# Optimization experiments

Measured on AMD Instinct MI355X. Metric: run time of the kernel, lower is better.

Reference implementation:

```python
import jax, jax.numpy as jnp
import numpy as np

B, S, D = 4, 4096, 1024
E, K, H = 8, 2, 2048


def setup_inputs() -> dict:
    key = jax.random.key(0)
    ks = jax.random.split(key, 6)
    scale_g = 1.0 / np.sqrt(D)
    scale_1 = 1.0 / np.sqrt(D)
    scale_2 = 1.0 / np.sqrt(H)
    return {
        "x": jax.random.normal(ks[0], (B, S, D), dtype=jnp.float32),
        "Wg": jax.random.uniform(ks[1], (D, E), jnp.float32, -scale_g, scale_g),
        "W1": jax.random.uniform(ks[2], (E, D, H), jnp.float32, -scale_1, scale_1),
        "b1": jax.random.uniform(ks[3], (E, H), jnp.float32, -scale_1, scale_1),
        "W2": jax.random.uniform(ks[4], (E, H, D), jnp.float32, -scale_2, scale_2),
        "b2": jax.random.uniform(ks[5], (E, D), jnp.float32, -scale_2, scale_2),
    }


def reference(x, Wg, W1, b1, W2, b2):
    # Router: softmax gate, top-k selection, renormalized combine weights
    logits = jnp.einsum("bsd,de->bse", x, Wg)          # [B,S,E]
    probs = jax.nn.softmax(logits, axis=-1)
    topv, topi = jax.lax.top_k(probs, K)                # [B,S,K]
    cw = topv / (jnp.sum(topv, axis=-1, keepdims=True) + 1e-9)
    # Per-token weight for each expert: sum over k of one_hot(idx_k)*cw_k -> [B,S,E]
    we = jnp.sum(jax.nn.one_hot(topi, E, dtype=x.dtype) * cw[..., None], axis=-2)
    # Weighted combine of per-expert FFN outputs (loop over small fixed E)
    y = jnp.zeros_like(x)
    for e in range(E):
        h = jax.nn.relu(jnp.einsum("bsd,dh->bsh", x, W1[e]) + b1[e])
        out_e = jnp.einsum("bsh,hd->bsd", h, W2[e]) + b2[e]
        y = y + we[..., e:e + 1] * out_e
    return y
```

## Files before the change

kernel.cpp:

```cpp
#include <hip/hip_runtime.h>
#include <hip/hip_bf16.h>

#define TOK 16384
#define DIM 1024
#define HID 2048
#define NEXP 8

typedef __attribute__((ext_vector_type(4))) float f32x4;
typedef __attribute__((ext_vector_type(8))) short s16x8;

__device__ __forceinline__ unsigned short f2bf(float f) {
  union { float f; unsigned u; } v; v.f = f;
  unsigned r = v.u + 0x7fffu + ((v.u >> 16) & 1u);
  return (unsigned short)(r >> 16);
}
__device__ __forceinline__ int tile_byte(int r, int kk2) {
  return (r * 128 + kk2) ^ ((r & 7) << 4);
}
__device__ __forceinline__ void gld_lds16(const void* g, void* l) {
  __builtin_amdgcn_global_load_lds(
      (const __attribute__((address_space(1))) unsigned int*)g,
      (__attribute__((address_space(3))) unsigned int*)l, 16, 0, 0);
}
__device__ __forceinline__ int xcd_swz(int p, int nwg) {
  int q = nwg >> 3, r = nwg & 7;
  int xcd = p & 7, idx = p >> 3;
  return (xcd < r ? xcd * (q + 1) : r * (q + 1) + (xcd - r) * q) + idx;
}

__global__ void wg_tr(const float* __restrict__ Wg, float* __restrict__ WgT) {
  int i = blockIdx.x * 256 + threadIdx.x;
  int e = i >> 10, dd = i & 1023;
  WgT[i] = Wg[dd * NEXP + e];
}

__global__ void prep_tiles(const float* __restrict__ src, unsigned short* __restrict__ dst,
                           int rows, int cols) {
  int ct = blockIdx.x, kb = blockIdx.y, e = blockIdx.z;
  int nct = gridDim.x, nkb = gridDim.y;
  __shared__ __align__(16) unsigned short tile[8192];
  const float* s = src + ((size_t)e * rows + kb * 64) * cols + ct * 128;
  int tid = threadIdx.x;
  #pragma unroll
  for (int it = 0; it < 8; it++) {
    int idx = it * 256 + tid;
    int kk = idx >> 5;
    int r4 = (idx & 31) * 4;
    float4 v = *(const float4*)(s + (size_t)kk * cols + r4);
    char* tb = (char*)tile;
    *(unsigned short*)(tb + tile_byte(r4 + 0, kk * 2)) = f2bf(v.x);
    *(unsigned short*)(tb + tile_byte(r4 + 1, kk * 2)) = f2bf(v.y);
    *(unsigned short*)(tb + tile_byte(r4 + 2, kk * 2)) = f2bf(v.z);
    *(unsigned short*)(tb + tile_byte(r4 + 3, kk * 2)) = f2bf(v.w);
  }
  __syncthreads();
  unsigned short* d = dst + (((size_t)e * nct + ct) * nkb + kb) * 8192;
  #pragma unroll
  for (int it = 0; it < 4; it++) {
    int o = it * 256 + tid;
    *(s16x8*)(d + o * 8) = *(const s16x8*)((const char*)tile + o * 16);
  }
}

__global__ __launch_bounds__(256)
void router_logits_cvt(const float* __restrict__ x, const float* __restrict__ WgT,
                       unsigned short* __restrict__ xbf,
                       int* __restrict__ sel, float2* __restrict__ wp) {
  int wave = threadIdx.x >> 6, lane = threadIdx.x & 63;
  int t = blockIdx.x * 4 + wave;
  const f32x4* xr = (const f32x4*)(x + (size_t)t * DIM);
  unsigned short* xb = xbf + (size_t)t * DIM;
  float acc[NEXP];
  #pragma unroll
  for (int e = 0; e < NEXP; e++) acc[e] = 0.f;
  #pragma unroll
  for (int q = 0; q < 4; q++) {
    f32x4 xv = xr[q * 64 + lane];
    ushort4 bv;
    bv.x = f2bf(xv[0]); bv.y = f2bf(xv[1]); bv.z = f2bf(xv[2]); bv.w = f2bf(xv[3]);
    *(ushort4*)(xb + (q * 64 + lane) * 4) = bv;
    #pragma unroll
    for (int e = 0; e < NEXP; e++) {
      f32x4 wv = *(const f32x4*)(WgT + (size_t)e * DIM + (q * 64 + lane) * 4);
      acc[e] = fmaf(xv[3], wv[3], fmaf(xv[2], wv[2], fmaf(xv[1], wv[1], fmaf(xv[0], wv[0], acc[e]))));
    }
  }
  #pragma unroll
  for (int e = 0; e < NEXP; e++) {
    float v = acc[e];
    #pragma unroll
    for (int off = 32; off >= 1; off >>= 1) v += __shfl_xor(v, off);
    acc[e] = v;
  }
  if (lane == 0) {
    float m = acc[0];
    #pragma unroll
    for (int e = 1; e < NEXP; e++) m = fmaxf(m, acc[e]);
    float p[NEXP], s = 0.f;
    #pragma unroll
    for (int e = 0; e < NEXP; e++) { p[e] = expf(acc[e] - m); s += p[e]; }
    float inv = 1.f / s;
    int i0 = 0; float v0 = p[0];
    #pragma unroll
    for (int e = 1; e < NEXP; e++) if (p[e] > v0) { v0 = p[e]; i0 = e; }
    int i1 = -1; float v1 = -1.f;
    #pragma unroll
    for (int e = 0; e < NEXP; e++) if (e != i0 && p[e] > v1) { v1 = p[e]; i1 = e; }
    v0 *= inv; v1 *= inv;
    float den = v0 + v1 + 1e-9f;
    sel[t] = i0 | (i1 << 4);
    wp[t] = make_float2(v0 / den, v1 / den);
  }
}

__global__ __launch_bounds__(256)
void router_scatter(const int* __restrict__ sel, const float2* __restrict__ wp,
                    int* __restrict__ counts, int* __restrict__ tok_list,
                    float* __restrict__ w_list) {
  __shared__ int lh0[4][16], lh1[4][16];
  __shared__ int bbase[16];
  int tid = threadIdx.x, wave = tid >> 6, lane = tid & 63;
  int t = blockIdx.x * 256 + tid;
  int s = sel[t];
  int b0 = s & 15;
  int b1 = 8 + ((s >> 4) & 15);
  float2 w = wp[t];
  unsigned long long lt = (lane == 63) ? ~0ull >> 1 : (((unsigned long long)1 << lane) - 1);
  int r0 = 0, r1 = 0;
  #pragma unroll
  for (int b = 0; b < 8; b++) {
    unsigned long long m0 = __ballot(b0 == b);
    if (b0 == b) r0 = __popcll(m0 & lt);
    if (lane == 0) { lh0[wave][b] = __popcll(m0); lh1[wave][b] = 0; }
  }
  #pragma unroll
  for (int b = 8; b < 16; b++) {
    unsigned long long m1 = __ballot(b1 == b);
    if (b1 == b) r1 = __popcll(m1 & lt);
    if (lane == 0) { lh1[wave][b] = __popcll(m1); lh0[wave][b] = 0; }
  }
  __syncthreads();
  if (tid < 16) {
    int h = 0;
    #pragma unroll
    for (int v = 0; v < 4; v++) h += lh0[v][tid] + lh1[v][tid];
    bbase[tid] = atomicAdd(&counts[tid], h);
  }
  __syncthreads();
  int p0 = bbase[b0] + r0;
  int p1 = bbase[b1] + r1;
  #pragma unroll
  for (int v = 0; v < 4; v++) {
    if (v < wave) { p0 += lh0[v][b0]; p1 += lh1[v][b1]; }
  }
  int e0 = b0, e1 = b1 - 8;
  tok_list[e0 * TOK + p0] = t;
  w_list[e0 * TOK + p0] = w.x;
  int q1 = TOK - 1 - p1;
  tok_list[e1 * TOK + q1] = t;
  w_list[e1 * TOK + q1] = w.y;
}

__global__ void calc_off(const int* __restrict__ counts, int* __restrict__ off) {
  if (threadIdx.x == 0 && blockIdx.x == 0) {
    int a = 0;
    for (int e = 0; e < NEXP; e++)
      for (int s = 0; s < 2; s++) {
        off[e * 2 + s] = a;
        a += (counts[s * 8 + e] + 127) & ~127;
      }
  }
}

__global__ __launch_bounds__(256, 4)
void moe_gemm1(const unsigned short* __restrict__ xbf, const unsigned short* __restrict__ w1s,
               const float* __restrict__ b1, const int* __restrict__ counts,
               const int* __restrict__ off, const int* __restrict__ tok_list,
               unsigned short* __restrict__ h_s, int ct_off, int nkbc, int nct) {
  int logical = xcd_swz(blockIdx.x, gridDim.x);
  int CG = (nct >= 8) ? 8 : nct;
  int e = -1, seg = 0, rt = 0, ct_l = 0, segcnt = 0, base = 0;
  #pragma unroll
  for (int zz = 0; zz < 16; zz++) {
    int ee = zz >> 1, ss = zz & 1;
    int c = counts[ss * 8 + ee];
    int nt = (c + 127) >> 7;
    int span = nt * nct;
    if (e < 0 && logical < base + span) {
      e = ee; seg = ss; segcnt = c;
      int local = logical - base;
      int grp = nt * CG;
      int h = local / grp, rem = local - h * grp;
      rt = rem / CG;
      ct_l = h * CG + (rem - rt * CG);
    }
    base += span;
  }
  if (e < 0) return;

  __shared__ __align__(16) unsigned short As[8192];
  __shared__ __align__(16) unsigned short Bs[8192];
  __shared__ int tokS[128];

  int tid = threadIdx.x, wave = tid >> 6, lane = tid & 63;
  int llo = lane & 15, lhi = lane >> 4;
  int wr = wave >> 1, wc = wave & 1;
  int ct_g = ct_off + ct_l;

  if (tid < 128) {
    int q = rt * 128 + tid;
    int qq = q < segcnt ? q : segcnt - 1;
    int slot = seg ? (TOK - 1 - qq) : qq;
    tokS[tid] = tok_list[e * TOK + slot];
  }
  __syncthreads();

  const char* srcA[4];
  #pragma unroll
  for (int i = 0; i < 4; i++) {
    int r = i * 32 + (tid >> 3);
    srcA[i] = (const char*)xbf + (size_t)tokS[r] * (DIM * 2) + (((tid & 7) ^ (r & 7)) * 16);
  }
  const char* gB = (const char*)(w1s + (((size_t)e * 16 + ct_g) * 16) * 8192);

  f32x4 acc[4][4];
  #pragma unroll
  for (int i = 0; i < 4; i++)
    #pragma unroll
    for (int j = 0; j < 4; j++) acc[i][j] = (f32x4){0.f, 0.f, 0.f, 0.f};

  for (int kb = 0; kb < 16; kb++) {
    #pragma unroll
    for (int i = 0; i < 4; i++)
      gld_lds16(srcA[i] + kb * 128, (char*)As + i * 4096 + wave * 1024);
    const char* gs = gB + (size_t)kb * 16384 + wave * 1024 + lane * 16;
    #pragma unroll
    for (int i = 0; i < 4; i++)
      gld_lds16(gs + i * 4096, (char*)Bs + i * 4096 + wave * 1024);
    __syncthreads();
    #pragma unroll
    for (int ks = 0; ks < 2; ks++) {
      s16x8 a[4], b[4];
      #pragma unroll
      for (int f = 0; f < 4; f++) {
        a[f] = *(const s16x8*)((const char*)As + tile_byte(wr * 64 + f * 16 + llo, ks * 64 + lhi * 16));
        b[f] = *(const s16x8*)((const char*)Bs + tile_byte(wc * 64 + f * 16 + llo, ks * 64 + lhi * 16));
      }
      #pragma unroll
      for (int fr = 0; fr < 4; fr++)
        #pragma unroll
        for (int fc = 0; fc < 4; fc++)
          acc[fr][fc] = __builtin_amdgcn_mfma_f32_16x16x32_bf16(a[fr], b[fc], acc[fr][fc], 0, 0, 0);
    }
    __syncthreads();
  }

  size_t grt = (size_t)(off[e * 2 + seg] >> 7) + rt;
  unsigned short* hb = h_s + grt * ((size_t)nkbc * 8192);
  const float* b1e = b1 + e * HID + ct_g * 128;
  #pragma unroll
  for (int fc = 0; fc < 4; fc++) {
    int col = wc * 64 + fc * 16 + llo;
    float bv = b1e[col];
    char* tb = (char*)(hb + ((size_t)(ct_l * 2 + (col >> 6))) * 8192);
    int kk2 = (col & 63) * 2;
    #pragma unroll
    for (int fr = 0; fr < 4; fr++) {
      int r0 = wr * 64 + fr * 16 + lhi * 4;
      #pragma unroll
      for (int j = 0; j < 4; j++) {
        float v = fmaxf(acc[fr][fc][j] + bv, 0.f);
        *(unsigned short*)(tb + tile_byte(r0 + j, kk2)) = f2bf(v);
      }
    }
  }
}

template<int NKBC>
__global__ __launch_bounds__(256, 4)
void moe_gemm2(const unsigned short* __restrict__ h_s, const unsigned short* __restrict__ w2s,
               const float* __restrict__ b2, const int* __restrict__ counts,
               const int* __restrict__ off, const int* __restrict__ tok_list,
               const float* __restrict__ w_list, float* __restrict__ y,
               int seg, int kb_off, int add_b2, int accum) {
  int logical = xcd_swz(blockIdx.x, gridDim.x);
  int e = -1, rt = 0, ct = 0, segcnt = 0, base = 0;
  #pragma unroll
  for (int ee = 0; ee < 8; ee++) {
    int c = counts[seg * 8 + ee];
    int nt = (c + 127) >> 7;
    int span = nt * 8;
    if (e < 0 && logical < base + span) {
      e = ee; segcnt = c;
      int local = logical - base;
      int grp = nt * 4;
      int h = local / grp, rem = local - h * grp;
      rt = rem >> 2;
      ct = h * 4 + (rem & 3);
    }
    base += span;
  }
  if (e < 0) return;

  __shared__ __align__(16) unsigned short As[8192];
  __shared__ __align__(16) unsigned short Bs[8192];

  int tid = threadIdx.x, wave = tid >> 6, lane = tid & 63;
  int llo = lane & 15, lhi = lane >> 4;
  int wr = wave >> 1, wc = wave & 1;

  size_t grt = (size_t)(off[e * 2 + seg] >> 7) + rt;
  const char* gA = (const char*)(h_s + grt * ((size_t)NKBC * 8192));
  const char* gB = (const char*)(w2s + (((size_t)e * 8 + ct) * 32 + kb_off) * 8192);

  f32x4 acc[4][4];
  #pragma unroll
  for (int i = 0; i < 4; i++)
    #pragma unroll
    for (int j = 0; j < 4; j++) acc[i][j] = (f32x4){0.f, 0.f, 0.f, 0.f};

  for (int kb = 0; kb < NKBC; kb++) {
    const char* ga = gA + (size_t)kb * 16384 + wave * 1024 + lane * 16;
    const char* gb = gB + (size_t)kb * 16384 + wave * 1024 + lane * 16;
    #pragma unroll
    for (int i = 0; i < 4; i++) {
      gld_lds16(ga + i * 4096, (char*)As + i * 4096 + wave * 1024);
      gld_lds16(gb + i * 4096, (char*)Bs + i * 4096 + wave * 1024);
    }
    __syncthreads();
    #pragma unroll
    for (int ks = 0; ks < 2; ks++) {
      s16x8 a[4], b[4];
      #pragma unroll
      for (int f = 0; f < 4; f++) {
        a[f] = *(const s16x8*)((const char*)As + tile_byte(wr * 64 + f * 16 + llo, ks * 64 + lhi * 16));
        b[f] = *(const s16x8*)((const char*)Bs + tile_byte(wc * 64 + f * 16 + llo, ks * 64 + lhi * 16));
      }
      #pragma unroll
      for (int fr = 0; fr < 4; fr++)
        #pragma unroll
        for (int fc = 0; fc < 4; fc++)
          acc[fr][fc] = __builtin_amdgcn_mfma_f32_16x16x32_bf16(a[fr], b[fc], acc[fr][fc], 0, 0, 0);
    }
    __syncthreads();
  }

  const float* b2e = b2 + e * DIM + ct * 128;
  #pragma unroll
  for (int fr = 0; fr < 4; fr++) {
    #pragma unroll
    for (int j = 0; j < 4; j++) {
      int q = rt * 128 + wr * 64 + fr * 16 + lhi * 4 + j;
      if (q < segcnt) {
        int slot = seg ? (TOK - 1 - q) : q;
        int t = tok_list[e * TOK + slot];
        float w = w_list[e * TOK + slot];
        float bs = add_b2 ? w : 0.f;
        #pragma unroll
        for (int fc = 0; fc < 4; fc++) {
          int col = wc * 64 + fc * 16 + llo;
          float val = w * acc[fr][fc][j] + bs * b2e[col];
          size_t idx = (size_t)t * DIM + ct * 128 + col;
          if (accum) y[idx] += val;
          else       y[idx] = val;
        }
      }
    }
  }
}

__global__ void transpose_cvt(const float* __restrict__ src, unsigned short* __restrict__ dst,
                              int R, int C) {
  __shared__ float tile[32][33];
  int e = blockIdx.z;
  const float* s = src + (size_t)e * R * C;
  unsigned short* d = dst + (size_t)e * R * C;
  int c0 = blockIdx.x * 32, r0 = blockIdx.y * 32;
  int tx = threadIdx.x, ty = threadIdx.y;
  #pragma unroll
  for (int i = 0; i < 32; i += 8)
    tile[ty + i][tx] = s[(size_t)(r0 + ty + i) * C + c0 + tx];
  __syncthreads();
  #pragma unroll
  for (int i = 0; i < 32; i += 8)
    d[(size_t)(c0 + ty + i) * R + r0 + tx] = f2bf(tile[tx][ty + i]);
}

__global__ void router_kernel(const float* __restrict__ x, const float* __restrict__ Wg,
                              int* __restrict__ counts, int* __restrict__ tok_list,
                              float* __restrict__ w_list) {
  int wave = threadIdx.x >> 6, lane = threadIdx.x & 63;
  int t = blockIdx.x * 4 + wave;
  const float* xr = x + (size_t)t * DIM;
  float acc[NEXP];
  #pragma unroll
  for (int e = 0; e < NEXP; e++) acc[e] = 0.f;
  for (int i = 0; i < DIM / 64; i++) {
    int dd = i * 64 + lane;
    float xv = xr[dd];
    const float* wr = Wg + (size_t)dd * NEXP;
    #pragma unroll
    for (int e = 0; e < NEXP; e++) acc[e] = fmaf(xv, wr[e], acc[e]);
  }
  #pragma unroll
  for (int e = 0; e < NEXP; e++) {
    float v = acc[e];
    #pragma unroll
    for (int off = 32; off >= 1; off >>= 1) v += __shfl_xor(v, off);
    acc[e] = v;
  }
  if (lane == 0) {
    float m = acc[0];
    #pragma unroll
    for (int e = 1; e < NEXP; e++) m = fmaxf(m, acc[e]);
    float p[NEXP], s = 0.f;
    #pragma unroll
    for (int e = 0; e < NEXP; e++) { p[e] = expf(acc[e] - m); s += p[e]; }
    float inv = 1.f / s;
    int i0 = 0; float v0 = p[0];
    #pragma unroll
    for (int e = 1; e < NEXP; e++) if (p[e] > v0) { v0 = p[e]; i0 = e; }
    int i1 = -1; float v1 = -1.f;
    #pragma unroll
    for (int e = 0; e < NEXP; e++) if (e != i0 && p[e] > v1) { v1 = p[e]; i1 = e; }
    v0 *= inv; v1 *= inv;
    float den = v0 + v1 + 1e-9f;
    float w0 = v0 / den, w1 = v1 / den;
    int q0 = atomicAdd(&counts[i0], 1);
    tok_list[i0 * TOK + q0] = t;           w_list[i0 * TOK + q0] = w0;
    int q1 = atomicAdd(&counts[8 + i1], 1);
    int p1 = TOK - 1 - q1;
    tok_list[i1 * TOK + p1] = t;           w_list[i1 * TOK + p1] = w1;
  }
}

__global__ __launch_bounds__(512, 4)
void moe_ffn_kernel(const float* __restrict__ x,
                    const unsigned short* __restrict__ w1t,
                    const unsigned short* __restrict__ w2t,
                    const float* __restrict__ b1, const float* __restrict__ b2,
                    const int* __restrict__ counts, const int* __restrict__ tok_list,
                    const float* __restrict__ w_list, float* __restrict__ y) {
  int zz = blockIdx.y, e = zz & 7, seg = zz >> 3;
  int segcnt = counts[seg * 8 + e];
  int row0 = blockIdx.x * 32;
  if (row0 >= segcnt) return;
  __shared__ unsigned short Xs[32 * DIM];
  __shared__ unsigned short hsl[32 * 64];
  __shared__ int tokS[32];
  __shared__ float wS[32];
  int tid = threadIdx.x, wave = tid >> 6, lane = tid & 63;
  if (tid < 32) {
    int q = row0 + tid;
    if (q < segcnt) {
      int slot = seg ? (TOK - 1 - q) : q;
      tokS[tid] = tok_list[e * TOK + slot]; wS[tid] = w_list[e * TOK + slot];
    } else { tokS[tid] = -1; wS[tid] = 0.f; }
  }
  __syncthreads();
  #pragma unroll
  for (int it = 0; it < 8; it++) {
    int chunk = it * 512 + tid;
    int r = chunk >> 7, c = (chunk & 127) * 8;
    int tok = tokS[r];
    float4 f0 = make_float4(0.f, 0.f, 0.f, 0.f), f1 = f0;
    if (tok >= 0) {
      const float4* xp = (const float4*)(x + (size_t)tok * DIM + c);
      f0 = xp[0]; f1 = xp[1];
    }
    s16x8 bv;
    bv[0] = (short)f2bf(f0.x); bv[1] = (short)f2bf(f0.y);
    bv[2] = (short)f2bf(f0.z); bv[3] = (short)f2bf(f0.w);
    bv[4] = (short)f2bf(f1.x); bv[5] = (short)f2bf(f1.y);
    bv[6] = (short)f2bf(f1.z); bv[7] = (short)f2bf(f1.w);
    int byte = (r * DIM + c) * 2; byte ^= (r & 7) << 4;
    *(s16x8*)((char*)Xs + byte) = bv;
  }
  __syncthreads();
  int rw = wave >> 2, cw = wave & 3;
  int lhi = lane >> 4, llo = lane & 15;
  f32x4 acc[16];
  #pragma unroll
  for (int i = 0; i < 16; i++) acc[i] = (f32x4){0.f, 0.f, 0.f, 0.f};
  int arow = rw * 16 + llo;
  int abase = arow * (DIM * 2) + lhi * 16;
  int aswz = (arow & 7) << 4;
  int h_abase = arow * (64 * 2) + lhi * 16;
  const size_t eHD = (size_t)e * HID * DIM;
  const unsigned short* w2e = w2t + (size_t)e * DIM * HID;
  for (int hc = 0; hc < HID; hc += 64) {
    f32x4 c1 = (f32x4){0.f, 0.f, 0.f, 0.f};
    const unsigned short* w1p = w1t + eHD + (size_t)(hc + cw * 16 + llo) * DIM + lhi * 8;
    #pragma unroll 4
    for (int k = 0; k < DIM; k += 32) {
      s16x8 a = *(const s16x8*)((const char*)Xs + ((abase + k * 2) ^ aswz));
      s16x8 b = *(const s16x8*)(w1p + k);
      c1 = __builtin_amdgcn_mfma_f32_16x16x32_bf16(a, b, c1, 0, 0, 0);
    }
    float b1v = b1[e * HID + hc + cw * 16 + llo];
    __syncthreads();
    #pragma unroll
    for (int j = 0; j < 4; j++) {
      int r = rw * 16 + lhi * 4 + j;
      float v = fmaxf(c1[j] + b1v, 0.f);
      int byte = (r * 64 + cw * 16 + llo) * 2; byte ^= (r & 7) << 4;
      *(unsigned short*)((char*)hsl + byte) = f2bf(v);
    }
    __syncthreads();
    s16x8 a0 = *(const s16x8*)((const char*)hsl + ((h_abase + 0)  ^ aswz));
    s16x8 a1 = *(const s16x8*)((const char*)hsl + ((h_abase + 64) ^ aswz));
    const unsigned short* w2p0 = w2e + hc + lhi * 8;
    #pragma unroll 4
    for (int ctile = 0; ctile < 16; ctile++) {
      int dcol = cw * 256 + ctile * 16 + llo;
      const unsigned short* bp = w2p0 + (size_t)dcol * HID;
      s16x8 b0 = *(const s16x8*)(bp);
      s16x8 b1f = *(const s16x8*)(bp + 32);
      acc[ctile] = __builtin_amdgcn_mfma_f32_16x16x32_bf16(a0, b0, acc[ctile], 0, 0, 0);
      acc[ctile] = __builtin_amdgcn_mfma_f32_16x16x32_bf16(a1, b1f, acc[ctile], 0, 0, 0);
    }
  }
  const float* b2e = b2 + e * DIM;
  #pragma unroll
  for (int ctile = 0; ctile < 16; ctile++) {
    int dcol = cw * 256 + ctile * 16 + llo;
    float b2v = b2e[dcol];
    #pragma unroll
    for (int j = 0; j < 4; j++) {
      int r = rw * 16 + lhi * 4 + j;
      int tok = tokS[r];
      if (tok >= 0) atomicAdd(&y[(size_t)tok * DIM + dcol], wS[r] * (acc[ctile][j] + b2v));
    }
  }
}

extern "C" void kernel_launch(void* const* d_in, const int* in_sizes, int n_in,
                              void* d_out, int out_size, void* d_ws, size_t ws_size,
                              hipStream_t stream) {
  const float* x  = (const float*)d_in[0];
  const float* Wg = (const float*)d_in[1];
  const float* W1 = (const float*)d_in[2];
  const float* b1 = (const float*)d_in[3];
  const float* W2 = (const float*)d_in[4];
  const float* b2 = (const float*)d_in[5];
  float* y = (float*)d_out;
  char* ws = (char*)d_ws;

  const size_t O_COUNTS = 0;
  const size_t O_OFF    = 1024;
  const size_t O_TOK    = 2048;
  const size_t O_W      = O_TOK + (size_t)NEXP * TOK * 4;
  const size_t O_WGT    = O_W + (size_t)NEXP * TOK * 4;
  const size_t O_SEL    = O_WGT + (size_t)NEXP * DIM * 4;
  const size_t O_WP     = O_SEL + (size_t)TOK * 4;
  const size_t O_W1S    = O_WP + (size_t)TOK * 8;
  const size_t O_W2S    = O_W1S + (size_t)NEXP * 16 * 16 * 8192 * 2;
  const size_t O_XBF    = O_W2S + (size_t)NEXP * 8 * 32 * 8192 * 2;
  const size_t O_HS     = O_XBF + (size_t)TOK * DIM * 2;

  int Hc = 0;
  if (ws_size > O_HS) {
    size_t avail = ws_size - O_HS;
    for (int hc = HID; hc >= 128; hc >>= 1)
      if ((size_t)34816 * hc * 2 <= avail) { Hc = hc; break; }
  }

  if (Hc) {
    int*   counts   = (int*)(ws + O_COUNTS);
    int*   offp     = (int*)(ws + O_OFF);
    int*   tok_list = (int*)(ws + O_TOK);
    float* w_list   = (float*)(ws + O_W);
    float* WgT      = (float*)(ws + O_WGT);
    int*   sel      = (int*)(ws + O_SEL);
    float2* wp      = (float2*)(ws + O_WP);
    unsigned short* w1s = (unsigned short*)(ws + O_W1S);
    unsigned short* w2s = (unsigned short*)(ws + O_W2S);
    unsigned short* xbf = (unsigned short*)(ws + O_XBF);
    unsigned short* hs  = (unsigned short*)(ws + O_HS);

    hipMemsetAsync(counts, 0, 2048, stream);
    wg_tr<<<32, 256, 0, stream>>>(Wg, WgT);
    prep_tiles<<<dim3(HID / 128, DIM / 64, NEXP), 256, 0, stream>>>(W1, w1s, DIM, HID);
    prep_tiles<<<dim3(DIM / 128, HID / 64, NEXP), 256, 0, stream>>>(W2, w2s, HID, DIM);
    router_logits_cvt<<<TOK / 4, 256, 0, stream>>>(x, WgT, xbf, sel, wp);
    router_scatter<<<TOK / 256, 256, 0, stream>>>(sel, wp, counts, tok_list, w_list);
    calc_off<<<1, 64, 0, stream>>>(counts, offp);

    int nch = HID / Hc, nkbc = Hc / 64, nct = Hc / 128;
    for (int ch = 0; ch < nch; ch++) {
      moe_gemm1<<<272 * nct, 256, 0, stream>>>(
          xbf, w1s, b1, counts, offp, tok_list, hs, ch * nct, nkbc, nct);
      for (int seg = 0; seg < 2; seg++) {
        int add_b2 = (ch == 0) ? 1 : 0;
        int accum  = (ch == 0 && seg == 0) ? 0 : 1;
        int kb_off = ch * nkbc;
        #define LG2(NK) moe_gemm2<NK><<<136 * 8, 256, 0, stream>>>( \
            hs, w2s, b2, counts, offp, tok_list, w_list, y, seg, kb_off, add_b2, accum)
        switch (nkbc) {
          case 32: LG2(32); break;
          case 16: LG2(16); break;
          case 8:  LG2(8);  break;
          case 4:  LG2(4);  break;
          default: LG2(2);  break;
        }
        #undef LG2
      }
    }
  } else {
    int*   counts   = (int*)ws;
    int*   tok_list = (int*)(ws + 2048);
    float* w_list   = (float*)(ws + 2048 + (size_t)NEXP * TOK * 4);
    unsigned short* w1t = (unsigned short*)(ws + 2048 + (size_t)NEXP * TOK * 8);
    unsigned short* w2t = w1t + (size_t)NEXP * HID * DIM;

    hipMemsetAsync(d_out, 0, (size_t)out_size * sizeof(float), stream);
    hipMemsetAsync(counts, 0, 2048, stream);
    transpose_cvt<<<dim3(HID / 32, DIM / 32, NEXP), dim3(32, 8), 0, stream>>>(W1, w1t, DIM, HID);
    transpose_cvt<<<dim3(DIM / 32, HID / 32, NEXP), dim3(32, 8), 0, stream>>>(W2, w2t, HID, DIM);
    router_kernel<<<TOK / 4, 256, 0, stream>>>(x, Wg, counts, tok_list, w_list);
    moe_ffn_kernel<<<dim3(TOK / 32, 16), 512, 0, stream>>>(
        x, w1t, w2t, b1, b2, counts, tok_list, w_list, y);
  }
}
```

Measured before the change: 505.1 us.

## Merge both top-k segments into one GEMM2 launch using a separate output buffer

```diff
diff --git a/kernel.cpp b/kernel.cpp
--- a/kernel.cpp
+++ b/kernel.cpp
@@ -172,6 +172,19 @@
   }
 }
 
+__global__ void combine_add(const float* __restrict__ y2, float* __restrict__ y) {
+  size_t n = (size_t)TOK * DIM / 4;
+  size_t stride = (size_t)gridDim.x * blockDim.x;
+  const f32x4* a = (const f32x4*)y2;
+  f32x4* o = (f32x4*)y;
+  for (size_t i = (size_t)blockIdx.x * blockDim.x + threadIdx.x; i < n; i += stride) {
+    f32x4 v = o[i], u = a[i];
+    #pragma unroll
+    for (int j = 0; j < 4; j++) v[j] += u[j];
+    o[i] = v;
+  }
+}
+
 __global__ __launch_bounds__(256, 4)
 void moe_gemm1(const unsigned short* __restrict__ xbf, const unsigned short* __restrict__ w1s,
                const float* __restrict__ b1, const int* __restrict__ counts,
@@ -271,6 +284,101 @@
       for (int j = 0; j < 4; j++) {
         float v = fmaxf(acc[fr][fc][j] + bv, 0.f);
         *(unsigned short*)(tb + tile_byte(r0 + j, kk2)) = f2bf(v);
+      }
+    }
+  }
+}
+
+template<int NKBC>
+__global__ __launch_bounds__(256, 4)
+void moe_gemm2b(const unsigned short* __restrict__ h_s, const unsigned short* __restrict__ w2s,
+                const float* __restrict__ b2, const int* __restrict__ counts,
+                const int* __restrict__ off, const int* __restrict__ tok_list,
+                const float* __restrict__ w_list, float* __restrict__ y,
+                float* __restrict__ y2, int kb_off, int add_b2, int accum) {
+  int logical = xcd_swz(blockIdx.x, gridDim.x);
+  int e = -1, seg = 0, rt = 0, ct = 0, segcnt = 0, base = 0;
+  #pragma unroll
+  for (int zz = 0; zz < 16; zz++) {
+    int ee = zz >> 1, ss = zz & 1;
+    int c = counts[ss * 8 + ee];
+    int nt = (c + 127) >> 7;
+    int span = nt * 8;
+    if (e < 0 && logical < base + span) {
+      e = ee; seg = ss; segcnt = c;
+      int local = logical - base;
+      int grp = nt * 4;
+      int h = local / grp, rem = local - h * grp;
+      rt = rem >> 2;
+      ct = h * 4 + (rem & 3);
+    }
+    base += span;
+  }
+  if (e < 0) return;
+  float* out = seg ? y2 : y;
+
+  __shared__ __align__(16) unsigned short As[8192];
+  __shared__ __align__(16) unsigned short Bs[8192];
+
+  int tid = threadIdx.x, wave = tid >> 6, lane = tid & 63;
+  int llo = lane & 15, lhi = lane >> 4;
+  int wr = wave >> 1, wc = wave & 1;
+
+  size_t grt = (size_t)(off[e * 2 + seg] >> 7) + rt;
+  const char* gA = (const char*)(h_s + grt * ((size_t)NKBC * 8192));
+  const char* gB = (const char*)(w2s + (((size_t)e * 8 + ct) * 32 + kb_off) * 8192);
+
+  f32x4 acc[4][4];
+  #pragma unroll
+  for (int i = 0; i < 4; i++)
+    #pragma unroll
+    for (int j = 0; j < 4; j++) acc[i][j] = (f32x4){0.f, 0.f, 0.f, 0.f};
+
+  for (int kb = 0; kb < NKBC; kb++) {
+    const char* ga = gA + (size_t)kb * 16384 + wave * 1024 + lane * 16;
+    const char* gb = gB + (size_t)kb * 16384 + wave * 1024 + lane * 16;
+    #pragma unroll
+    for (int i = 0; i < 4; i++) {
+      gld_lds16(ga + i * 4096, (char*)As + i * 4096 + wave * 1024);
+      gld_lds16(gb + i * 4096, (char*)Bs + i * 4096 + wave * 1024);
+    }
+    __syncthreads();
+    #pragma unroll
+    for (int ks = 0; ks < 2; ks++) {
+      s16x8 a[4], b[4];
+      #pragma unroll
+      for (int f = 0; f < 4; f++) {
+        a[f] = *(const s16x8*)((const char*)As + tile_byte(wr * 64 + f * 16 + llo, ks * 64 + lhi * 16));
+        b[f] = *(const s16x8*)((const char*)Bs + tile_byte(wc * 64 + f * 16 + llo, ks * 64 + lhi * 16));
+      }
+      #pragma unroll
+      for (int fr = 0; fr < 4; fr++)
+        #pragma unroll
+        for (int fc = 0; fc < 4; fc++)
+          acc[fr][fc] = __builtin_amdgcn_mfma_f32_16x16x32_bf16(a[fr], b[fc], acc[fr][fc], 0, 0, 0);
+    }
+    __syncthreads();
+  }
+
+  const float* b2e = b2 + e * DIM + ct * 128;
+  #pragma unroll
+  for (int fr = 0; fr < 4; fr++) {
+    #pragma unroll
+    for (int j = 0; j < 4; j++) {
+      int q = rt * 128 + wr * 64 + fr * 16 + lhi * 4 + j;
+      if (q < segcnt) {
+        int slot = seg ? (TOK - 1 - q) : q;
+        int t = tok_list[e * TOK + slot];
+        float w = w_list[e * TOK + slot];
+        float bs = add_b2 ? w : 0.f;
+        #pragma unroll
+        for (int fc = 0; fc < 4; fc++) {
+          int col = wc * 64 + fc * 16 + llo;
+          float val = w * acc[fr][fc][j] + bs * b2e[col];
+          size_t idx = (size_t)t * DIM + ct * 128 + col;
+          if (accum) out[idx] += val;
+          else       out[idx] = val;
+        }
       }
     }
   }
@@ -556,16 +664,24 @@
   const size_t O_W1S    = O_WP + (size_t)TOK * 8;
   const size_t O_W2S    = O_W1S + (size_t)NEXP * 16 * 16 * 8192 * 2;
   const size_t O_XBF    = O_W2S + (size_t)NEXP * 8 * 32 * 8192 * 2;
-  const size_t O_HS     = O_XBF + (size_t)TOK * DIM * 2;
+  const size_t O_Y2     = O_XBF + (size_t)TOK * DIM * 2;
+  const size_t O_HS_Y2  = O_Y2 + (size_t)TOK * DIM * 4;
+  const size_t O_HS_OLD = O_Y2;
 
   int Hc = 0;
-  if (ws_size > O_HS) {
-    size_t avail = ws_size - O_HS;
+  if (ws_size > O_HS_Y2) {
+    size_t avail = ws_size - O_HS_Y2;
     for (int hc = HID; hc >= 128; hc >>= 1)
       if ((size_t)34816 * hc * 2 <= avail) { Hc = hc; break; }
   }
-
-  if (Hc) {
+  int HcOld = 0;
+  if (!Hc && ws_size > O_HS_OLD) {
+    size_t avail = ws_size - O_HS_OLD;
+    for (int hc = HID; hc >= 128; hc >>= 1)
+      if ((size_t)34816 * hc * 2 <= avail) { HcOld = hc; break; }
+  }
+
+  if (Hc || HcOld) {
     int*   counts   = (int*)(ws + O_COUNTS);
     int*   offp     = (int*)(ws + O_OFF);
     int*   tok_list = (int*)(ws + O_TOK);
@@ -576,7 +692,8 @@
     unsigned short* w1s = (unsigned short*)(ws + O_W1S);
     unsigned short* w2s = (unsigned short*)(ws + O_W2S);
     unsigned short* xbf = (unsigned short*)(ws + O_XBF);
-    unsigned short* hs  = (unsigned short*)(ws + O_HS);
+    float*          y2f = (float*)(ws + O_Y2);
+    unsigned short* hs  = (unsigned short*)(ws + (Hc ? O_HS_Y2 : O_HS_OLD));
 
     hipMemsetAsync(counts, 0, 2048, stream);
     wg_tr<<<32, 256, 0, stream>>>(Wg, WgT);
@@ -586,24 +703,44 @@
     router_scatter<<<TOK / 256, 256, 0, stream>>>(sel, wp, counts, tok_list, w_list);
     calc_off<<<1, 64, 0, stream>>>(counts, offp);
 
-    int nch = HID / Hc, nkbc = Hc / 64, nct = Hc / 128;
-    for (int ch = 0; ch < nch; ch++) {
-      moe_gemm1<<<272 * nct, 256, 0, stream>>>(
-          xbf, w1s, b1, counts, offp, tok_list, hs, ch * nct, nkbc, nct);
-      for (int seg = 0; seg < 2; seg++) {
+    if (Hc) {
+      int nch = HID / Hc, nkbc = Hc / 64, nct = Hc / 128;
+      for (int ch = 0; ch < nch; ch++) {
+        moe_gemm1<<<272 * nct, 256, 0, stream>>>(
+            xbf, w1s, b1, counts, offp, tok_list, hs, ch * nct, nkbc, nct);
         int add_b2 = (ch == 0) ? 1 : 0;
-        int accum  = (ch == 0 && seg == 0) ? 0 : 1;
-        int kb_off = ch * nkbc;
-        #define LG2(NK) moe_gemm2<NK><<<136 * 8, 256, 0, stream>>>( \
-            hs, w2s, b2, counts, offp, tok_list, w_list, y, seg, kb_off, add_b2, accum)
+        int accum  = (ch == 0) ? 0 : 1;
+        #define LG2B(NK) moe_gemm2b<NK><<<2176, 256, 0, stream>>>( \
+            hs, w2s, b2, counts, offp, tok_list, w_list, y, y2f, ch * nkbc, add_b2, accum)
         switch (nkbc) {
-          case 32: LG2(32); break;
-          case 16: LG2(16); break;
-          case 8:  LG2(8);  break;
-          case 4:  LG2(4);  break;
-          default: LG2(2);  break;
+          case 32: LG2B(32); break;
+          case 16: LG2B(16); break;
+          case 8:  LG2B(8);  break;
+          case 4:  LG2B(4);  break;
+          default: LG2B(2);  break;
         }
-        #undef LG2
+        #undef LG2B
+      }
+      combine_add<<<2048, 256, 0, stream>>>(y2f, y);
+    } else {
+      int nch = HID / HcOld, nkbc = HcOld / 64, nct = HcOld / 128;
+      for (int ch = 0; ch < nch; ch++) {
+        moe_gemm1<<<272 * nct, 256, 0, stream>>>(
+            xbf, w1s, b1, counts, offp, tok_list, hs, ch * nct, nkbc, nct);
+        for (int seg = 0; seg < 2; seg++) {
+          int add_b2 = (ch == 0) ? 1 : 0;
+          int accum  = (ch == 0 && seg == 0) ? 0 : 1;
+          #define LG2(NK) moe_gemm2<NK><<<136 * 8, 256, 0, stream>>>( \
+              hs, w2s, b2, counts, offp, tok_list, w_list, y, seg, ch * nkbc, add_b2, accum)
+          switch (nkbc) {
+            case 32: LG2(32); break;
+            case 16: LG2(16); break;
+            case 8:  LG2(8);  break;
+            case 4:  LG2(4);  break;
+            default: LG2(2);  break;
+          }
+          #undef LG2
+        }
       }
     }
   } else {
```

After: 604.1 us. 1.2x slower.

## Widen GEMM2 tiles to 128x256 with 8 waves and triple-buffered async loads

Applied to the files above, without the earlier changes.

```diff
diff --git a/kernel.cpp b/kernel.cpp
--- a/kernel.cpp
+++ b/kernel.cpp
@@ -277,41 +277,41 @@
 }
 
 template<int NKBC>
-__global__ __launch_bounds__(256, 4)
-void moe_gemm2(const unsigned short* __restrict__ h_s, const unsigned short* __restrict__ w2s,
-               const float* __restrict__ b2, const int* __restrict__ counts,
-               const int* __restrict__ off, const int* __restrict__ tok_list,
-               const float* __restrict__ w_list, float* __restrict__ y,
-               int seg, int kb_off, int add_b2, int accum) {
+__global__ __launch_bounds__(512, 1)
+void moe_gemm2p(const unsigned short* __restrict__ h_s, const unsigned short* __restrict__ w2s,
+                const float* __restrict__ b2, const int* __restrict__ counts,
+                const int* __restrict__ off, const int* __restrict__ tok_list,
+                const float* __restrict__ w_list, float* __restrict__ y,
+                int seg, int kb_off, int add_b2, int accum) {
   int logical = xcd_swz(blockIdx.x, gridDim.x);
-  int e = -1, rt = 0, ct = 0, segcnt = 0, base = 0;
+  int e = -1, rt = 0, ctp = 0, segcnt = 0, base = 0;
   #pragma unroll
   for (int ee = 0; ee < 8; ee++) {
     int c = counts[seg * 8 + ee];
     int nt = (c + 127) >> 7;
-    int span = nt * 8;
+    int span = nt * 4;
     if (e < 0 && logical < base + span) {
       e = ee; segcnt = c;
       int local = logical - base;
-      int grp = nt * 4;
+      int grp = nt * 2;
       int h = local / grp, rem = local - h * grp;
-      rt = rem >> 2;
-      ct = h * 4 + (rem & 3);
+      rt = rem >> 1;
+      ctp = h * 2 + (rem & 1);
     }
     base += span;
   }
   if (e < 0) return;
 
-  __shared__ __align__(16) unsigned short As[8192];
-  __shared__ __align__(16) unsigned short Bs[8192];
+  __shared__ __align__(16) unsigned short S[3 * 24576];
 
   int tid = threadIdx.x, wave = tid >> 6, lane = tid & 63;
   int llo = lane & 15, lhi = lane >> 4;
-  int wr = wave >> 1, wc = wave & 1;
+  int wr = wave >> 2, wc = wave & 3;
 
   size_t grt = (size_t)(off[e * 2 + seg] >> 7) + rt;
-  const char* gA = (const char*)(h_s + grt * ((size_t)NKBC * 8192));
-  const char* gB = (const char*)(w2s + (((size_t)e * 8 + ct) * 32 + kb_off) * 8192);
+  const char* gA  = (const char*)(h_s + grt * ((size_t)NKBC * 8192));
+  const char* gB0 = (const char*)(w2s + (((size_t)e * 8 + ctp * 2) * 32 + kb_off) * 8192);
+  const char* gB1 = gB0 + (size_t)32 * 16384;
 
   f32x4 acc[4][4];
   #pragma unroll
@@ -319,22 +319,42 @@
     #pragma unroll
     for (int j = 0; j < 4; j++) acc[i][j] = (f32x4){0.f, 0.f, 0.f, 0.f};
 
-  for (int kb = 0; kb < NKBC; kb++) {
-    const char* ga = gA + (size_t)kb * 16384 + wave * 1024 + lane * 16;
-    const char* gb = gB + (size_t)kb * 16384 + wave * 1024 + lane * 16;
-    #pragma unroll
-    for (int i = 0; i < 4; i++) {
-      gld_lds16(ga + i * 4096, (char*)As + i * 4096 + wave * 1024);
-      gld_lds16(gb + i * 4096, (char*)Bs + i * 4096 + wave * 1024);
-    }
-    __syncthreads();
+  auto stage = [&](int h) {
+    char* ls = (char*)S + (h % 3) * 49152;
+    const char* ga  = gA  + (size_t)h * 16384;
+    const char* gb0 = gB0 + (size_t)h * 16384;
+    const char* gb1 = gB1 + (size_t)h * 16384;
+    #pragma unroll
+    for (int i = 0; i < 2; i++) {
+      gld_lds16(ga  + i * 8192 + tid * 16, ls +         i * 8192 + tid * 16);
+      gld_lds16(gb0 + i * 8192 + tid * 16, ls + 16384 + i * 8192 + tid * 16);
+      gld_lds16(gb1 + i * 8192 + tid * 16, ls + 32768 + i * 8192 + tid * 16);
+    }
+  };
+
+  stage(0);
+  if (NKBC > 1) stage(1);
+  for (int h = 0; h < NKBC; h++) {
+    if (h + 2 < NKBC) {
+      stage(h + 2);
+      asm volatile("s_waitcnt vmcnt(12)" ::: "memory");
+    } else if (h + 1 < NKBC) {
+      asm volatile("s_waitcnt vmcnt(6)" ::: "memory");
+    } else {
+      asm volatile("s_waitcnt vmcnt(0)" ::: "memory");
+    }
+    __builtin_amdgcn_s_barrier();
+    __builtin_amdgcn_sched_barrier(0);
+    const char* As_ = (const char*)S + (h % 3) * 49152;
+    const char* Bs_ = As_ + 16384 + ((wc >> 1) ? 16384 : 0);
+    int bc = (wc & 1) * 64;
     #pragma unroll
     for (int ks = 0; ks < 2; ks++) {
       s16x8 a[4], b[4];
       #pragma unroll
       for (int f = 0; f < 4; f++) {
-        a[f] = *(const s16x8*)((const char*)As + tile_byte(wr * 64 + f * 16 + llo, ks * 64 + lhi * 16));
-        b[f] = *(const s16x8*)((const char*)Bs + tile_byte(wc * 64 + f * 16 + llo, ks * 64 + lhi * 16));
+        a[f] = *(const s16x8*)(As_ + tile_byte(wr * 64 + f * 16 + llo, ks * 64 + lhi * 16));
+        b[f] = *(const s16x8*)(Bs_ + tile_byte(bc + f * 16 + llo, ks * 64 + lhi * 16));
       }
       #pragma unroll
       for (int fr = 0; fr < 4; fr++)
@@ -342,10 +362,11 @@
         for (int fc = 0; fc < 4; fc++)
           acc[fr][fc] = __builtin_amdgcn_mfma_f32_16x16x32_bf16(a[fr], b[fc], acc[fr][fc], 0, 0, 0);
     }
-    __syncthreads();
-  }
-
-  const float* b2e = b2 + e * DIM + ct * 128;
+    __builtin_amdgcn_sched_barrier(0);
+    __builtin_amdgcn_s_barrier();
+  }
+
+  const float* b2e = b2 + e * DIM + ctp * 256;
   #pragma unroll
   for (int fr = 0; fr < 4; fr++) {
     #pragma unroll
@@ -358,9 +379,9 @@
         float bs = add_b2 ? w : 0.f;
         #pragma unroll
         for (int fc = 0; fc < 4; fc++) {
-          int col = wc * 64 + fc * 16 + llo;
-          float val = w * acc[fr][fc][j] + bs * b2e[col];
-          size_t idx = (size_t)t * DIM + ct * 128 + col;
+          int lcol = wc * 64 + fc * 16 + llo;
+          float val = w * acc[fr][fc][j] + bs * b2e[lcol];
+          size_t idx = (size_t)t * DIM + ctp * 256 + lcol;
           if (accum) y[idx] += val;
           else       y[idx] = val;
         }
@@ -594,16 +615,16 @@
         int add_b2 = (ch == 0) ? 1 : 0;
         int accum  = (ch == 0 && seg == 0) ? 0 : 1;
         int kb_off = ch * nkbc;
-        #define LG2(NK) moe_gemm2<NK><<<136 * 8, 256, 0, stream>>>( \
+        #define LG2P(NK) moe_gemm2p<NK><<<136 * 4, 512, 0, stream>>>( \
             hs, w2s, b2, counts, offp, tok_list, w_list, y, seg, kb_off, add_b2, accum)
         switch (nkbc) {
-          case 32: LG2(32); break;
-          case 16: LG2(16); break;
-          case 8:  LG2(8);  break;
-          case 4:  LG2(4);  break;
-          default: LG2(2);  break;
+          case 32: LG2P(32); break;
+          case 16: LG2P(16); break;
+          case 8:  LG2P(8);  break;
+          case 4:  LG2P(4);  break;
+          default: LG2P(2);  break;
         }
-        #undef LG2
+        #undef LG2P
       }
     }
   } else {
```

New measurement: 574.7 us. +13.8%, slower.

## Enlarge GEMM2 tiles to 256x256 with double-buffered LDS and 8 waves

Applied to the files above, without the earlier changes.

```diff
diff --git a/kernel.cpp b/kernel.cpp
--- a/kernel.cpp
+++ b/kernel.cpp
@@ -277,90 +277,142 @@
 }
 
 template<int NKBC>
-__global__ __launch_bounds__(256, 4)
-void moe_gemm2(const unsigned short* __restrict__ h_s, const unsigned short* __restrict__ w2s,
-               const float* __restrict__ b2, const int* __restrict__ counts,
-               const int* __restrict__ off, const int* __restrict__ tok_list,
-               const float* __restrict__ w_list, float* __restrict__ y,
-               int seg, int kb_off, int add_b2, int accum) {
+__global__ __launch_bounds__(512, 1)
+void moe_gemm2q(const unsigned short* __restrict__ h_s, const unsigned short* __restrict__ w2s,
+                const float* __restrict__ b2, const int* __restrict__ counts,
+                const int* __restrict__ off, const int* __restrict__ tok_list,
+                const float* __restrict__ w_list, float* __restrict__ y,
+                int seg, int kb_off, int add_b2, int accum) {
   int logical = xcd_swz(blockIdx.x, gridDim.x);
-  int e = -1, rt = 0, ct = 0, segcnt = 0, base = 0;
+  int e = -1, rt2 = 0, ct2 = 0, segcnt = 0, ntl = 0, base = 0;
   #pragma unroll
   for (int ee = 0; ee < 8; ee++) {
     int c = counts[seg * 8 + ee];
     int nt = (c + 127) >> 7;
-    int span = nt * 8;
+    int mt = (nt + 1) >> 1;
+    int span = mt * 4;
     if (e < 0 && logical < base + span) {
-      e = ee; segcnt = c;
+      e = ee; segcnt = c; ntl = nt;
       int local = logical - base;
-      int grp = nt * 4;
-      int h = local / grp, rem = local - h * grp;
-      rt = rem >> 2;
-      ct = h * 4 + (rem & 3);
+      rt2 = local >> 2;
+      ct2 = local & 3;
     }
     base += span;
   }
   if (e < 0) return;
 
-  __shared__ __align__(16) unsigned short As[8192];
-  __shared__ __align__(16) unsigned short Bs[8192];
+  __shared__ __align__(16) char S[2][65536];
 
   int tid = threadIdx.x, wave = tid >> 6, lane = tid & 63;
   int llo = lane & 15, lhi = lane >> 4;
-  int wr = wave >> 1, wc = wave & 1;
-
-  size_t grt = (size_t)(off[e * 2 + seg] >> 7) + rt;
-  const char* gA = (const char*)(h_s + grt * ((size_t)NKBC * 8192));
-  const char* gB = (const char*)(w2s + (((size_t)e * 8 + ct) * 32 + kb_off) * 8192);
-
-  f32x4 acc[4][4];
-  #pragma unroll
-  for (int i = 0; i < 4; i++)
+  int wr2 = wave >> 2;
+  int wc4 = wave & 3;
+
+  int grt0 = (off[e * 2 + seg] >> 7) + rt2 * 2;
+  int grt1 = grt0 + ((rt2 * 2 + 1 < ntl) ? 1 : 0);
+  const char* pA[2] = {
+    (const char*)(h_s + (size_t)grt0 * NKBC * 8192),
+    (const char*)(h_s + (size_t)grt1 * NKBC * 8192) };
+  const char* pB[2] = {
+    (const char*)(w2s + (((size_t)e * 8 + ct2 * 2 + 0) * 32 + kb_off) * 8192),
+    (const char*)(w2s + (((size_t)e * 8 + ct2 * 2 + 1) * 32 + kb_off) * 8192) };
+
+  f32x4 acc[8][4];
+  #pragma unroll
+  for (int i = 0; i < 8; i++)
     #pragma unroll
     for (int j = 0; j < 4; j++) acc[i][j] = (f32x4){0.f, 0.f, 0.f, 0.f};
 
+  {
+    char* Dst = S[0];
+    #pragma unroll
+    for (int c = 0; c < 4; c++)
+      gld_lds16(pA[c >> 1] + (c & 1) * 8192 + tid * 16, Dst + c * 8192 + tid * 16);
+    #pragma unroll
+    for (int c = 0; c < 4; c++)
+      gld_lds16(pB[c >> 1] + (c & 1) * 8192 + tid * 16, Dst + 32768 + c * 8192 + tid * 16);
+  }
+  __syncthreads();
+
   for (int kb = 0; kb < NKBC; kb++) {
-    const char* ga = gA + (size_t)kb * 16384 + wave * 1024 + lane * 16;
-    const char* gb = gB + (size_t)kb * 16384 + wave * 1024 + lane * 16;
-    #pragma unroll
-    for (int i = 0; i < 4; i++) {
-      gld_lds16(ga + i * 4096, (char*)As + i * 4096 + wave * 1024);
-      gld_lds16(gb + i * 4096, (char*)Bs + i * 4096 + wave * 1024);
-    }
-    __syncthreads();
-    #pragma unroll
-    for (int ks = 0; ks < 2; ks++) {
-      s16x8 a[4], b[4];
-      #pragma unroll
-      for (int f = 0; f < 4; f++) {
-        a[f] = *(const s16x8*)((const char*)As + tile_byte(wr * 64 + f * 16 + llo, ks * 64 + lhi * 16));
-        b[f] = *(const s16x8*)((const char*)Bs + tile_byte(wc * 64 + f * 16 + llo, ks * 64 + lhi * 16));
-      }
-      #pragma unroll
-      for (int fr = 0; fr < 4; fr++)
+    int cur = kb & 1;
+    const char* Atile = S[cur] + wr2 * 16384;
+    const char* Btile = S[cur] + 32768 + (wc4 >> 1) * 16384;
+    int bro = (wc4 & 1) * 64;
+
+    s16x8 bfr[4][2], afr[2][2];
+    #pragma unroll
+    for (int n = 0; n < 4; n++)
+      #pragma unroll
+      for (int ks = 0; ks < 2; ks++)
+        bfr[n][ks] = *(const s16x8*)(Btile + tile_byte(bro + n * 16 + llo, ks * 64 + lhi * 16));
+    #pragma unroll
+    for (int mm = 0; mm < 2; mm++)
+      #pragma unroll
+      for (int ks = 0; ks < 2; ks++)
+        afr[mm][ks] = *(const s16x8*)(Atile + tile_byte(mm * 16 + llo, ks * 64 + lhi * 16));
+    if (kb + 1 < NKBC) {
+      char* Dst = S[cur ^ 1];
+      size_t ko = (size_t)(kb + 1) * 16384;
+      #pragma unroll
+      for (int c = 0; c < 4; c++)
+        gld_lds16(pA[c >> 1] + ko + (c & 1) * 8192 + tid * 16, Dst + c * 8192 + tid * 16);
+      #pragma unroll
+      for (int c = 0; c < 4; c++)
+        gld_lds16(pB[c >> 1] + ko + (c & 1) * 8192 + tid * 16, Dst + 32768 + c * 8192 + tid * 16);
+    }
+    asm volatile("s_waitcnt lgkmcnt(0)" ::: "memory");
+    __builtin_amdgcn_sched_barrier(0);
+    __builtin_amdgcn_s_setprio(1);
+    #pragma unroll
+    for (int mm = 0; mm < 2; mm++)
+      #pragma unroll
+      for (int n = 0; n < 4; n++)
         #pragma unroll
-        for (int fc = 0; fc < 4; fc++)
-          acc[fr][fc] = __builtin_amdgcn_mfma_f32_16x16x32_bf16(a[fr], b[fc], acc[fr][fc], 0, 0, 0);
-    }
-    __syncthreads();
-  }
-
-  const float* b2e = b2 + e * DIM + ct * 128;
-  #pragma unroll
-  for (int fr = 0; fr < 4; fr++) {
+        for (int ks = 0; ks < 2; ks++)
+          acc[mm][n] = __builtin_amdgcn_mfma_f32_16x16x32_bf16(afr[mm][ks], bfr[n][ks], acc[mm][n], 0, 0, 0);
+    __builtin_amdgcn_s_setprio(0);
+
+    #pragma unroll
+    for (int p = 1; p < 4; p++) {
+      #pragma unroll
+      for (int mm = 0; mm < 2; mm++)
+        #pragma unroll
+        for (int ks = 0; ks < 2; ks++)
+          afr[mm][ks] = *(const s16x8*)(Atile + tile_byte((2 * p + mm) * 16 + llo, ks * 64 + lhi * 16));
+      asm volatile("s_waitcnt lgkmcnt(0)" ::: "memory");
+      __builtin_amdgcn_sched_barrier(0);
+      __builtin_amdgcn_s_setprio(1);
+      #pragma unroll
+      for (int mm = 0; mm < 2; mm++)
+        #pragma unroll
+        for (int n = 0; n < 4; n++)
+          #pragma unroll
+          for (int ks = 0; ks < 2; ks++)
+            acc[2 * p + mm][n] = __builtin_amdgcn_mfma_f32_16x16x32_bf16(afr[mm][ks], bfr[n][ks], acc[2 * p + mm][n], 0, 0, 0);
+      __builtin_amdgcn_s_setprio(0);
+    }
+
+    asm volatile("s_waitcnt vmcnt(0)" ::: "memory");
+    __builtin_amdgcn_s_barrier();
+  }
+
+  const float* b2e = b2 + e * DIM + ct2 * 256;
+  #pragma unroll
+  for (int m = 0; m < 8; m++) {
     #pragma unroll
     for (int j = 0; j < 4; j++) {
-      int q = rt * 128 + wr * 64 + fr * 16 + lhi * 4 + j;
+      int q = rt2 * 256 + wr2 * 128 + m * 16 + lhi * 4 + j;
       if (q < segcnt) {
         int slot = seg ? (TOK - 1 - q) : q;
         int t = tok_list[e * TOK + slot];
         float w = w_list[e * TOK + slot];
         float bs = add_b2 ? w : 0.f;
         #pragma unroll
-        for (int fc = 0; fc < 4; fc++) {
-          int col = wc * 64 + fc * 16 + llo;
-          float val = w * acc[fr][fc][j] + bs * b2e[col];
-          size_t idx = (size_t)t * DIM + ct * 128 + col;
+        for (int n = 0; n < 4; n++) {
+          int col = wc4 * 64 + n * 16 + llo;
+          float val = w * acc[m][n][j] + bs * b2e[col];
+          size_t idx = (size_t)t * DIM + ct2 * 256 + col;
           if (accum) y[idx] += val;
           else       y[idx] = val;
         }
@@ -594,16 +646,16 @@
         int add_b2 = (ch == 0) ? 1 : 0;
         int accum  = (ch == 0 && seg == 0) ? 0 : 1;
         int kb_off = ch * nkbc;
-        #define LG2(NK) moe_gemm2<NK><<<136 * 8, 256, 0, stream>>>( \
+        #define LG2Q(NK) moe_gemm2q<NK><<<288, 512, 0, stream>>>( \
             hs, w2s, b2, counts, offp, tok_list, w_list, y, seg, kb_off, add_b2, accum)
         switch (nkbc) {
-          case 32: LG2(32); break;
-          case 16: LG2(16); break;
-          case 8:  LG2(8);  break;
-          case 4:  LG2(4);  break;
-          default: LG2(2);  break;
+          case 32: LG2Q(32); break;
+          case 16: LG2Q(16); break;
+          case 8:  LG2Q(8);  break;
+          case 4:  LG2Q(4);  break;
+          default: LG2Q(2);  break;
         }
-        #undef LG2
+        #undef LG2Q
       }
     }
   } else {
```

Measured after the change: 610.3 us. 1.21x slower.
